# Performance work log

Measured on AMD Instinct MI355X. Metric: run time of the kernel, lower is better.

## Reference

```python
import jax, jax.numpy as jnp
import numpy as np

B, T, N, C = 2, 8, 10242, 64
K, NBR, O = 9, 7, 64


def setup_inputs() -> dict:
    key = jax.random.key(0)
    k1, k2, k3, k4, k5 = jax.random.split(key, 5)
    x = jax.random.normal(k1, (B, T, N, C), dtype=jnp.float32)
    index = jax.random.randint(k2, (N, NBR), 0, N, dtype=jnp.int64)
    itp_mat = jax.random.uniform(k3, (N, NBR, K), dtype=jnp.float32)
    conv_w = jax.random.normal(k4, (O, C, 1, K), dtype=jnp.float32) * (1.0 / np.sqrt(C * K))
    conv_b = jax.random.normal(k5, (O,), dtype=jnp.float32) * 0.01
    return {"x": x, "index": index, "itp_mat": itp_mat, "conv_w": conv_w, "conv_b": conv_b}


def reference(x, index, itp_mat, conv_w, conv_b):
    b, t, n, c = x.shape
    o = conv_w.shape[0]
    # (B,T,N,C) -> (B*T, C, N)
    feats = x.reshape(b * t, n, c).transpose(0, 2, 1)
    # gather neighbors: (BT, C, N, NBR)
    nb = feats[:, :, index]
    # per-node interpolation matmul: (BT, C, N, K)
    itp = jnp.einsum('bcnj,njk->bcnk', nb, itp_mat)
    # Conv2d with kernel (1,K) on width K collapses K fully: (BT, O, N)
    out = jnp.einsum('bcnk,ock->bon', itp, conv_w[:, :, 0, :]) + conv_b[None, :, None]
    # (B, T, O, N) -> (B, T, N, O)
    return out.reshape(b, t, o, n).transpose(0, 1, 3, 2)
```

## Files before the change

### kernel.cpp

```cpp
#include <hip/hip_runtime.h>

#define BT    16
#define NN    10242
#define CC    64
#define KK    9
#define NBR_  7
#define OO    64
#define CK    576
#define MT    16
#define RS    584
#define KT    18

using frag  = __attribute__((ext_vector_type(8))) short;
using f32x4 = __attribute__((ext_vector_type(4))) float;

static __device__ __forceinline__ unsigned short f2bf(float f) {
    union { float f; unsigned u; } v; v.f = f;
    unsigned r = v.u + 0x7fffu + ((v.u >> 16) & 1u);
    return (unsigned short)(r >> 16);
}

__global__ void pack_w_kernel(const float* __restrict__ w, unsigned short* __restrict__ wb) {
    int i = blockIdx.x * blockDim.x + threadIdx.x;
    if (i >= KT * 4 * 64 * 8) return;
    int j  = i & 7;
    int l  = (i >> 3) & 63;
    int ct = (i >> 9) & 3;
    int t  = i >> 11;
    int q  = t * 32 + (l >> 4) * 8 + j;
    int o  = ct * 16 + (l & 15);
    int c, k;
    if (q < 512) { c = (q & 255) >> 2; k = (q >> 8) * 4 + (q & 3); }
    else         { c = q - 512;        k = 8; }
    wb[i] = f2bf(w[(o * CC + c) * KK + k]);
}

__global__ __launch_bounds__(256, 8) void sphere_conv_kernel(
    const float* __restrict__ x,
    const int*   __restrict__ index,
    const float* __restrict__ m,
    const unsigned short* __restrict__ wb,
    const float* __restrict__ bias,
    float*       __restrict__ out)
{
    __shared__ unsigned short itp_s[MT * RS];

    const int tid  = threadIdx.x;
    const int nt   = blockIdx.x;
    const int bt   = blockIdx.y;
    const int n0   = nt * MT;
    const int w    = tid >> 6;
    const int lane = tid & 63;

    {
        const float* xbt = x + (size_t)bt * NN * CC;

        int nu[4];
        #pragma unroll
        for (int r = 0; r < 4; ++r) {
            const int n = n0 + w * 4 + r;
            nu[r] = __builtin_amdgcn_readfirstlane(n < NN ? n : (NN - 1));
        }

        float xv[4][NBR_];
        #pragma unroll
        for (int r = 0; r < 4; ++r) {
            const int* ip = index + nu[r] * NBR_;
            #pragma unroll
            for (int j = 0; j < NBR_; ++j)
                xv[r][j] = xbt[(size_t)ip[j] * CC + lane];
        }

        #pragma unroll
        for (int r = 0; r < 4; ++r) {
            const int ns = w * 4 + r;
            const float* mp = m + nu[r] * (NBR_ * KK);
            float acc[KK];
            #pragma unroll
            for (int k = 0; k < KK; ++k) acc[k] = 0.f;
            #pragma unroll
            for (int j = 0; j < NBR_; ++j)
                #pragma unroll
                for (int k = 0; k < KK; ++k)
                    acc[k] = fmaf(xv[r][j], mp[j * KK + k], acc[k]);

            unsigned short h[KK];
            #pragma unroll
            for (int k = 0; k < KK; ++k) h[k] = f2bf(acc[k]);
            uint2 q0, q1;
            q0.x = (unsigned)h[0] | ((unsigned)h[1] << 16);
            q0.y = (unsigned)h[2] | ((unsigned)h[3] << 16);
            q1.x = (unsigned)h[4] | ((unsigned)h[5] << 16);
            q1.y = (unsigned)h[6] | ((unsigned)h[7] << 16);
            unsigned short* row = &itp_s[ns * RS];
            *(uint2*)(&row[lane * 4])       = q0;
            *(uint2*)(&row[256 + lane * 4]) = q1;
            row[512 + lane] = h[8];
        }
    }
    __syncthreads();

    const int ct   = w;
    const int am   = lane & 15;
    const int half = lane >> 4;

    f32x4 acc = (f32x4){0.f, 0.f, 0.f, 0.f};

    const unsigned short* arow = &itp_s[am * RS + half * 8];
    const frag* wbf = (const frag*)wb;

    #pragma unroll
    for (int t = 0; t < KT; ++t) {
        const frag a = *(const frag*)(arow + t * 32);
        const frag b = wbf[(t * 4 + ct) * 64 + lane];
        acc = __builtin_amdgcn_mfma_f32_16x16x32_bf16(a, b, acc, 0, 0, 0);
    }

    const size_t obase = (size_t)bt * NN * OO;
    {
        const int o  = ct * 16 + am;
        const float bo = bias[o];
        #pragma unroll
        for (int i = 0; i < 4; ++i) {
            const int n = n0 + half * 4 + i;
            if (n < NN) out[obase + (size_t)n * OO + o] = acc[i] + bo;
        }
    }
}

extern "C" void kernel_launch(void* const* d_in, const int* in_sizes, int n_in,
                              void* d_out, int out_size, void* d_ws, size_t ws_size,
                              hipStream_t stream) {
    const float* x      = (const float*)d_in[0];
    const int*   index  = (const int*)  d_in[1];
    const float* m      = (const float*)d_in[2];
    const float* conv_w = (const float*)d_in[3];
    const float* conv_b = (const float*)d_in[4];
    float* out = (float*)d_out;
    unsigned short* wb = (unsigned short*)d_ws;

    {
        const int total = KT * 4 * 64 * 8;
        pack_w_kernel<<<(total + 255) / 256, 256, 0, stream>>>(conv_w, wb);
    }
    {
        dim3 grid((NN + MT - 1) / MT, BT);
        sphere_conv_kernel<<<grid, 256, 0, stream>>>(x, index, m, wb, conv_b, out);
    }
}
```

Measured before the change: 147.3 us.

## Process two node tiles per block with double-buffered LDS and XCD-aware mapping

Each block now handles two consecutive 16-node tiles using two LDS buffers, so producing the second tile (gathers plus interpolation) can overlap the MFMA consume of the first. The packed conv weights are hoisted into registers once per block, and the bias load is also hoisted. A 1D grid remaps block ids so that each XCD processes two BT slices, aiming for better L2 locality of gathered x rows. The costs are more registers (launch bounds drop to 4 waves/SIMD), twice the LDS, and half as many blocks.

```diff
diff --git a/kernel.cpp b/kernel.cpp
--- a/kernel.cpp
+++ b/kernel.cpp
@@ -1,15 +1,17 @@
 #include <hip/hip_runtime.h>
 
-#define BT    16
-#define NN    10242
-#define CC    64
-#define KK    9
-#define NBR_  7
-#define OO    64
-#define CK    576
-#define MT    16
-#define RS    584
-#define KT    18
+#define BT     16
+#define NN     10242
+#define CC     64
+#define KK     9
+#define NBR_   7
+#define OO     64
+#define CK     576
+#define MT     16
+#define RS     584
+#define KT     18
+#define NTILES 641
+#define NGRP   321
 
 using frag  = __attribute__((ext_vector_type(8))) short;
 using f32x4 = __attribute__((ext_vector_type(4))) float;
@@ -35,7 +37,75 @@
     wb[i] = f2bf(w[(o * CC + c) * KK + k]);
 }
 
-__global__ __launch_bounds__(256, 8) void sphere_conv_kernel(
+static __device__ __forceinline__ void produce_tile(
+    const float* __restrict__ xbt, const int* __restrict__ index,
+    const float* __restrict__ m, unsigned short* __restrict__ buf,
+    int n0, int w, int lane)
+{
+    int nu[4];
+    #pragma unroll
+    for (int r = 0; r < 4; ++r) {
+        const int n = n0 + w * 4 + r;
+        nu[r] = __builtin_amdgcn_readfirstlane(n < NN ? n : (NN - 1));
+    }
+    float xv[4][NBR_];
+    #pragma unroll
+    for (int r = 0; r < 4; ++r) {
+        const int* ip = index + nu[r] * NBR_;
+        #pragma unroll
+        for (int j = 0; j < NBR_; ++j)
+            xv[r][j] = xbt[(size_t)ip[j] * CC + lane];
+    }
+    #pragma unroll
+    for (int r = 0; r < 4; ++r) {
+        const int ns = w * 4 + r;
+        const float* mp = m + nu[r] * (NBR_ * KK);
+        float acc[KK];
+        #pragma unroll
+        for (int k = 0; k < KK; ++k) acc[k] = 0.f;
+        #pragma unroll
+        for (int j = 0; j < NBR_; ++j)
+            #pragma unroll
+            for (int k = 0; k < KK; ++k)
+                acc[k] = fmaf(xv[r][j], mp[j * KK + k], acc[k]);
+
+        unsigned short h[KK];
+        #pragma unroll
+        for (int k = 0; k < KK; ++k) h[k] = f2bf(acc[k]);
+        uint2 q0, q1;
+        q0.x = (unsigned)h[0] | ((unsigned)h[1] << 16);
+        q0.y = (unsigned)h[2] | ((unsigned)h[3] << 16);
+        q1.x = (unsigned)h[4] | ((unsigned)h[5] << 16);
+        q1.y = (unsigned)h[6] | ((unsigned)h[7] << 16);
+        unsigned short* row = &buf[ns * RS];
+        *(uint2*)(&row[lane * 4])       = q0;
+        *(uint2*)(&row[256 + lane * 4]) = q1;
+        row[512 + lane] = h[8];
+    }
+}
+
+static __device__ __forceinline__ void consume_tile(
+    const unsigned short* __restrict__ buf, const frag* __restrict__ bfr,
+    float* __restrict__ out, size_t obase, int n0, int w, int lane, float bo)
+{
+    const int am   = lane & 15;
+    const int half = lane >> 4;
+    const int o    = w * 16 + am;
+    const unsigned short* arow = &buf[am * RS + half * 8];
+    f32x4 acc = (f32x4){0.f, 0.f, 0.f, 0.f};
+    #pragma unroll
+    for (int t = 0; t < KT; ++t) {
+        const frag a = *(const frag*)(arow + t * 32);
+        acc = __builtin_amdgcn_mfma_f32_16x16x32_bf16(a, bfr[t], acc, 0, 0, 0);
+    }
+    #pragma unroll
+    for (int i = 0; i < 4; ++i) {
+        const int n = n0 + half * 4 + i;
+        if (n < NN) out[obase + (size_t)n * OO + o] = acc[i] + bo;
+    }
+}
+
+__global__ __launch_bounds__(256, 4) void sphere_conv_kernel(
     const float* __restrict__ x,
     const int*   __restrict__ index,
     const float* __restrict__ m,
@@ -43,88 +113,40 @@
     const float* __restrict__ bias,
     float*       __restrict__ out)
 {
-    __shared__ unsigned short itp_s[MT * RS];
+    __shared__ unsigned short itp_s[2][MT * RS];
 
     const int tid  = threadIdx.x;
-    const int nt   = blockIdx.x;
-    const int bt   = blockIdx.y;
-    const int n0   = nt * MT;
     const int w    = tid >> 6;
     const int lane = tid & 63;
 
-    {
-        const float* xbt = x + (size_t)bt * NN * CC;
+    const int bid  = blockIdx.x;
+    const int xcd  = bid & 7;
+    const int slot = bid >> 3;
+    const int btl  = slot / NGRP;
+    const int g    = slot - btl * NGRP;
+    const int bt   = xcd * 2 + btl;
+    const int n00  = (g * 2) * MT;
+    const int n01  = n00 + MT;
+    const bool has1 = (g * 2 + 1) < NTILES;
 
-        int nu[4];
-        #pragma unroll
-        for (int r = 0; r < 4; ++r) {
-            const int n = n0 + w * 4 + r;
-            nu[r] = __builtin_amdgcn_readfirstlane(n < NN ? n : (NN - 1));
-        }
+    const float* xbt = x + (size_t)bt * NN * CC;
+    const size_t obase = (size_t)bt * NN * OO;
 
-        float xv[4][NBR_];
-        #pragma unroll
-        for (int r = 0; r < 4; ++r) {
-            const int* ip = index + nu[r] * NBR_;
-            #pragma unroll
-            for (int j = 0; j < NBR_; ++j)
-                xv[r][j] = xbt[(size_t)ip[j] * CC + lane];
-        }
+    const frag* wbf = (const frag*)wb;
+    frag bfr[KT];
+    #pragma unroll
+    for (int t = 0; t < KT; ++t) bfr[t] = wbf[(t * 4 + w) * 64 + lane];
 
-        #pragma unroll
-        for (int r = 0; r < 4; ++r) {
-            const int ns = w * 4 + r;
-            const float* mp = m + nu[r] * (NBR_ * KK);
-            float acc[KK];
-            #pragma unroll
-            for (int k = 0; k < KK; ++k) acc[k] = 0.f;
-            #pragma unroll
-            for (int j = 0; j < NBR_; ++j)
-                #pragma unroll
-                for (int k = 0; k < KK; ++k)
-                    acc[k] = fmaf(xv[r][j], mp[j * KK + k], acc[k]);
+    const float bo = bias[w * 16 + (lane & 15)];
 
-            unsigned short h[KK];
-            #pragma unroll
-            for (int k = 0; k < KK; ++k) h[k] = f2bf(acc[k]);
-            uint2 q0, q1;
-            q0.x = (unsigned)h[0] | ((unsigned)h[1] << 16);
-            q0.y = (unsigned)h[2] | ((unsigned)h[3] << 16);
-            q1.x = (unsigned)h[4] | ((unsigned)h[5] << 16);
-            q1.y = (unsigned)h[6] | ((unsigned)h[7] << 16);
-            unsigned short* row = &itp_s[ns * RS];
-            *(uint2*)(&row[lane * 4])       = q0;
-            *(uint2*)(&row[256 + lane * 4]) = q1;
-            row[512 + lane] = h[8];
-        }
-    }
+    produce_tile(xbt, index, m, itp_s[0], n00, w, lane);
     __syncthreads();
 
-    const int ct   = w;
-    const int am   = lane & 15;
-    const int half = lane >> 4;
-
-    f32x4 acc = (f32x4){0.f, 0.f, 0.f, 0.f};
-
-    const unsigned short* arow = &itp_s[am * RS + half * 8];
-    const frag* wbf = (const frag*)wb;
-
-    #pragma unroll
-    for (int t = 0; t < KT; ++t) {
-        const frag a = *(const frag*)(arow + t * 32);
-        const frag b = wbf[(t * 4 + ct) * 64 + lane];
-        acc = __builtin_amdgcn_mfma_f32_16x16x32_bf16(a, b, acc, 0, 0, 0);
-    }
-
-    const size_t obase = (size_t)bt * NN * OO;
-    {
-        const int o  = ct * 16 + am;
-        const float bo = bias[o];
-        #pragma unroll
-        for (int i = 0; i < 4; ++i) {
-            const int n = n0 + half * 4 + i;
-            if (n < NN) out[obase + (size_t)n * OO + o] = acc[i] + bo;
-        }
+    if (has1) produce_tile(xbt, index, m, itp_s[1], n01, w, lane);
+    consume_tile(itp_s[0], bfr, out, obase, n00, w, lane, bo);
+    if (has1) {
+        __syncthreads();
+        consume_tile(itp_s[1], bfr, out, obase, n01, w, lane, bo);
     }
 }
 
@@ -144,7 +166,7 @@
         pack_w_kernel<<<(total + 255) / 256, 256, 0, stream>>>(conv_w, wb);
     }
     {
-        dim3 grid((NN + MT - 1) / MT, BT);
+        dim3 grid(8 * 2 * NGRP);
         sphere_conv_kernel<<<grid, 256, 0, stream>>>(x, index, m, wb, conv_b, out);
     }
 }
```

Result: slower. 169.8 us (+15.2%).
